# Kernel tuning notes

Measured on AMD Instinct MI355X. Metric: run time of the kernel, lower is better.

## Reference

```python
import jax, jax.numpy as jnp
import numpy as np

DIM = 1024
HEADS = 16
HEAD_DIM = DIM // HEADS
SCALE = HEAD_DIM ** -0.5


def setup_inputs() -> dict:
    key = jax.random.key(0)
    ks = jax.random.split(key, 6)
    B, N, C = 2, 2048, DIM
    q = jax.random.normal(ks[0], (B, N, C), dtype=jnp.float32)
    k = jax.random.normal(ks[1], (B, N, C), dtype=jnp.float32)
    v = jax.random.normal(ks[2], (B, N, C), dtype=jnp.float32)
    # torch nn.Linear weights: out = x @ W.T (+ b); qkv has no bias (qkv_bias=False)
    W_qkv = jax.random.normal(ks[3], (3 * C, 3 * C), dtype=jnp.float32) * (3 * C) ** -0.5
    W_proj = jax.random.normal(ks[4], (C, C), dtype=jnp.float32) * C ** -0.5
    b_proj = jax.random.normal(ks[5], (C,), dtype=jnp.float32) * 0.02
    return {"q": q, "k": k, "v": v, "W_qkv": W_qkv, "W_proj": W_proj, "b_proj": b_proj}


def reference(q, k, v, W_qkv, W_proj, b_proj):
    B, N, C = q.shape
    # fused QKV projection on concatenated [q,k,v] -> [B,N,3C]
    qkv = jnp.concatenate([q, k, v], axis=-1) @ W_qkv.T
    qkv = qkv.reshape(B, N, 3, HEADS, HEAD_DIM).transpose(2, 0, 3, 1, 4)  # [3,B,H,N,hd]
    qh, kh, vh = qkv[0], qkv[1], qkv[2]
    attn = jnp.einsum('bhqd,bhkd->bhqk', qh, kh) * SCALE
    attn = jax.nn.softmax(attn, axis=-1)  # attn_drop is identity (p=0)
    x = jnp.einsum('bhqk,bhkd->bhqd', attn, vh)  # [B,H,N,hd]
    x = x.transpose(0, 2, 1, 3).reshape(B, N, C)
    x = x @ W_proj.T + b_proj  # proj_drop is identity (p=0)
    return x
```

## Files before the change

### kernel.cpp

```cpp
#include <hip/hip_runtime.h>
#include <hip/hip_bf16.h>
#include <stdint.h>

#define HEADS 16
#define HD 64
#define SEQ 2048
#define BATCH 2
#define CDIM 1024
#define MROWS (BATCH*SEQ)
#define K3C (3*CDIM)
#define ATT_SCALE 0.125f

typedef __bf16 bf16x8 __attribute__((ext_vector_type(8)));
typedef float  f32x4  __attribute__((ext_vector_type(4)));

__device__ __forceinline__ unsigned short f2bf(float f) {
    __hip_bfloat16 h = __float2bfloat16(f);
    return __builtin_bit_cast(unsigned short, h);
}
__device__ __forceinline__ unsigned int pack2bf(float a, float b) {
    return (unsigned int)f2bf(a) | ((unsigned int)f2bf(b) << 16);
}
__device__ __forceinline__ bf16x8 frag(uint4 u) { return __builtin_bit_cast(bf16x8, u); }

__device__ __forceinline__ void async16(const unsigned short* g, unsigned short* lds) {
    __builtin_amdgcn_global_load_lds(
        (const __attribute__((address_space(1))) unsigned int*)g,
        (__attribute__((address_space(3))) unsigned int*)lds, 16, 0, 0);
}

__global__ void cast_all(const float* __restrict__ q, const float* __restrict__ k,
                         const float* __restrict__ v, const float* __restrict__ Wq,
                         const float* __restrict__ Wp,
                         unsigned short* __restrict__ A, unsigned short* __restrict__ Wqb,
                         unsigned short* __restrict__ Wpb)
{
    const int bid = blockIdx.x;
    const int t = threadIdx.x;
    if (bid < MROWS) {
        const float* srcs[3] = {q, k, v};
        #pragma unroll
        for (int i = 0; i < 3; ++i) {
            float4 f = *(const float4*)(srcs[i] + (size_t)bid*CDIM + t*4);
            ushort4 s;
            s.x = f2bf(f.x); s.y = f2bf(f.y); s.z = f2bf(f.z); s.w = f2bf(f.w);
            *(ushort4*)(A + (size_t)bid*K3C + i*CDIM + t*4) = s;
        }
    } else if (bid < MROWS + 9216) {
        int idx = (bid - MROWS)*256 + t;
        float4 f = ((const float4*)Wq)[idx];
        ushort4 s;
        s.x = f2bf(f.x); s.y = f2bf(f.y); s.z = f2bf(f.z); s.w = f2bf(f.w);
        ((ushort4*)Wqb)[idx] = s;
    } else {
        int idx = (bid - MROWS - 9216)*256 + t;
        float4 f = ((const float4*)Wp)[idx];
        ushort4 s;
        s.x = f2bf(f.x); s.y = f2bf(f.y); s.z = f2bf(f.z); s.w = f2bf(f.w);
        ((ushort4*)Wpb)[idx] = s;
    }
}

template<int EPI>
__global__ __launch_bounds__(256, 2)
void gemm_bt(const unsigned short* __restrict__ A, const unsigned short* __restrict__ B,
             int M, int N, int K,
             unsigned short* __restrict__ qh, unsigned short* __restrict__ kh,
             unsigned short* __restrict__ vt,
             const float* __restrict__ bias, float* __restrict__ out)
{
    __shared__ __attribute__((aligned(16))) unsigned short As[128*32];
    __shared__ __attribute__((aligned(16))) unsigned short Bs[128*32];
    const int tid  = threadIdx.x;
    const int wave = tid >> 6;
    const int lane = tid & 63;
    const int l15  = lane & 15;
    const int quad = lane >> 4;
    const int wm = (wave >> 1) * 64;
    const int wn = (wave & 1) * 64;
    const int m0 = blockIdx.x * 128;
    const int n0 = blockIdx.y * 128;

    f32x4 acc[4][4] = {};

    const int srow = tid >> 2;
    const int sc8  = (tid & 3) * 8;

    for (int k0 = 0; k0 < K; k0 += 32) {
        #pragma unroll
        for (int t = 0; t < 2; ++t) {
            int row = t*64 + srow;
            const unsigned short* ga = A + (size_t)(m0 + row)*K + k0 + sc8;
            const unsigned short* gb = B + (size_t)(n0 + row)*K + k0 + sc8;
            async16(ga, &As[(t*256 + wave*64)*8]);
            async16(gb, &Bs[(t*256 + wave*64)*8]);
        }
        __syncthreads();
        uint4 af[4], bfv[4];
        #pragma unroll
        for (int i = 0; i < 4; ++i) {
            af[i]  = *(const uint4*)&As[(wm + i*16 + l15)*32 + quad*8];
            bfv[i] = *(const uint4*)&Bs[(wn + i*16 + l15)*32 + quad*8];
        }
        #pragma unroll
        for (int mi = 0; mi < 4; ++mi)
            #pragma unroll
            for (int ni = 0; ni < 4; ++ni)
                acc[mi][ni] = __builtin_amdgcn_mfma_f32_16x16x32_bf16(
                    frag(af[mi]), frag(bfv[ni]), acc[mi][ni], 0, 0, 0);
        __syncthreads();
    }

    if constexpr (EPI == 0) {
        #pragma unroll
        for (int mi = 0; mi < 4; ++mi) {
            int row0 = m0 + wm + mi*16 + quad*4;
            int b  = row0 >> 11;
            int nq = row0 & 2047;
            #pragma unroll
            for (int ni = 0; ni < 4; ++ni) {
                int col   = n0 + wn + ni*16 + l15;
                int which = col >> 10;
                int h     = (col >> 6) & 15;
                int d     = col & 63;
                int bh    = b*HEADS + h;
                if (which == 2) {
                    ushort4 pv;
                    pv.x = f2bf(acc[mi][ni][0]);
                    pv.y = f2bf(acc[mi][ni][1]);
                    pv.z = f2bf(acc[mi][ni][2]);
                    pv.w = f2bf(acc[mi][ni][3]);
                    *(ushort4*)&vt[((size_t)bh*HD + d)*SEQ + nq] = pv;
                } else {
                    unsigned short* dst = (which == 0) ? qh : kh;
                    float sc = (which == 0) ? ATT_SCALE : 1.0f;
                    #pragma unroll
                    for (int r = 0; r < 4; ++r)
                        dst[((size_t)bh*SEQ + nq + r)*HD + d] = f2bf(acc[mi][ni][r] * sc);
                }
            }
        }
    } else {
        #pragma unroll
        for (int mi = 0; mi < 4; ++mi) {
            int row0 = m0 + wm + mi*16 + quad*4;
            #pragma unroll
            for (int ni = 0; ni < 4; ++ni) {
                int col  = n0 + wn + ni*16 + l15;
                float bv = bias[col];
                #pragma unroll
                for (int r = 0; r < 4; ++r)
                    out[(size_t)(row0 + r)*N + col] = acc[mi][ni][r] + bv;
            }
        }
    }
}

__global__ __launch_bounds__(256, 2)
void attention(const unsigned short* __restrict__ qh, const unsigned short* __restrict__ kh,
               const unsigned short* __restrict__ vt, unsigned short* __restrict__ xb)
{
    const int qt = blockIdx.x;
    const int h  = blockIdx.y;
    const int b  = blockIdx.z;
    const int bh = b*HEADS + h;
    const int tid  = threadIdx.x;
    const int wave = tid >> 6;
    const int lane = tid & 63;
    const int l15  = lane & 15;
    const int quad = lane >> 4;

    __shared__ __attribute__((aligned(16))) unsigned short Ks[2][64*64];
    __shared__ __attribute__((aligned(16))) unsigned short Vs[2][64*64];
    __shared__ __attribute__((aligned(16))) unsigned short Ps[4][16*72];

    const unsigned short* Qp = qh + ((size_t)bh*SEQ + qt*64)*HD;
    const unsigned short* Kp = kh + (size_t)bh*SEQ*HD;
    const unsigned short* Vp = vt + (size_t)bh*HD*SEQ;

    auto stage = [&](int kt, int bufI) {
        #pragma unroll
        for (int t = 0; t < 2; ++t) {
            int c  = t*256 + wave*64 + lane;
            int r  = c >> 3;
            int cc = (c & 7) ^ (r & 7);
            async16(Kp + (size_t)(kt*64 + r)*HD + cc*8,
                    &Ks[bufI][(t*256 + wave*64)*8]);
            async16(Vp + (size_t)r*SEQ + kt*64 + cc*8,
                    &Vs[bufI][(t*256 + wave*64)*8]);
        }
    };

    uint4 qf0 = *(const uint4*)(Qp + (size_t)(wave*16 + l15)*HD + quad*8);
    uint4 qf1 = *(const uint4*)(Qp + (size_t)(wave*16 + l15)*HD + 32 + quad*8);

    f32x4 o[4] = {};
    float m_s = -INFINITY, l_s = 0.f;

    unsigned short* Pl = Ps[wave];
    const int x7 = l15 & 7;

    stage(0, 0);

    for (int kt = 0; kt < SEQ/64; ++kt) {
        stage((kt + 1) & 31, (kt + 1) & 1);
        asm volatile("s_waitcnt vmcnt(4)" ::: "memory");
        asm volatile("s_barrier" ::: "memory");

        const unsigned short* Kb = Ks[kt & 1];
        const unsigned short* Vb = Vs[kt & 1];

        f32x4 s[4];
        #pragma unroll
        for (int st = 0; st < 4; ++st) {
            int rb = st*16 + l15;
            uint4 kf0 = *(const uint4*)&Kb[(rb*8 + (quad ^ x7))*8];
            uint4 kf1 = *(const uint4*)&Kb[(rb*8 + ((4 + quad) ^ x7))*8];
            f32x4 z = {};
            z = __builtin_amdgcn_mfma_f32_16x16x32_bf16(frag(kf0), frag(qf0), z, 0, 0, 0);
            z = __builtin_amdgcn_mfma_f32_16x16x32_bf16(frag(kf1), frag(qf1), z, 0, 0, 0);
            s[st] = z;
        }

        float mloc = s[0][0];
        #pragma unroll
        for (int st = 0; st < 4; ++st)
            #pragma unroll
            for (int r = 0; r < 4; ++r)
                mloc = fmaxf(mloc, s[st][r]);
        mloc = fmaxf(mloc, __shfl_xor(mloc, 16));
        mloc = fmaxf(mloc, __shfl_xor(mloc, 32));

        float mn = fmaxf(m_s, mloc);
        float al = __expf(m_s - mn);
        m_s = mn;

        float p[4][4];
        float rs = 0.f;
        #pragma unroll
        for (int st = 0; st < 4; ++st)
            #pragma unroll
            for (int r = 0; r < 4; ++r) { p[st][r] = __expf(s[st][r] - mn); rs += p[st][r]; }
        rs += __shfl_xor(rs, 16);
        rs += __shfl_xor(rs, 32);
        l_s = al*l_s + rs;

        #pragma unroll
        for (int st = 0; st < 4; ++st)
            #pragma unroll
            for (int r = 0; r < 4; ++r)
                o[st][r] *= al;

        #pragma unroll
        for (int st = 0; st < 4; ++st) {
            uint2 pk;
            pk.x = pack2bf(p[st][0], p[st][1]);
            pk.y = pack2bf(p[st][2], p[st][3]);
            *(uint2*)&Pl[l15*72 + st*16 + quad*4] = pk;
        }
        asm volatile("s_waitcnt lgkmcnt(0)" ::: "memory");

        uint4 pB0 = *(const uint4*)&Pl[l15*72 + quad*8];
        uint4 pB1 = *(const uint4*)&Pl[l15*72 + 32 + quad*8];

        #pragma unroll
        for (int st = 0; st < 4; ++st) {
            int rb = st*16 + l15;
            uint4 vf0 = *(const uint4*)&Vb[(rb*8 + (quad ^ x7))*8];
            uint4 vf1 = *(const uint4*)&Vb[(rb*8 + ((4 + quad) ^ x7))*8];
            o[st] = __builtin_amdgcn_mfma_f32_16x16x32_bf16(frag(vf0), frag(pB0), o[st], 0, 0, 0);
            o[st] = __builtin_amdgcn_mfma_f32_16x16x32_bf16(frag(vf1), frag(pB1), o[st], 0, 0, 0);
        }

        asm volatile("s_barrier" ::: "memory");
    }

    float inv = 1.0f / l_s;
    #pragma unroll
    for (int st = 0; st < 4; ++st) {
        uint2 pk;
        pk.x = pack2bf(o[st][0]*inv, o[st][1]*inv);
        pk.y = pack2bf(o[st][2]*inv, o[st][3]*inv);
        *(uint2*)&Pl[l15*72 + st*16 + quad*4] = pk;
    }
    asm volatile("s_waitcnt lgkmcnt(0)" ::: "memory");
    __syncthreads();

    const int qr = lane >> 2;
    const int dd = (lane & 3) * 16;
    uint4 oa = *(const uint4*)&Pl[qr*72 + dd];
    uint4 ob = *(const uint4*)&Pl[qr*72 + dd + 8];
    const int mrow = b*SEQ + qt*64 + wave*16 + qr;
    *(uint4*)&xb[(size_t)mrow*CDIM + h*HD + dd]     = oa;
    *(uint4*)&xb[(size_t)mrow*CDIM + h*HD + dd + 8] = ob;
}

extern "C" void kernel_launch(void* const* d_in, const int* in_sizes, int n_in,
                              void* d_out, int out_size, void* d_ws, size_t ws_size,
                              hipStream_t stream)
{
    const float* q  = (const float*)d_in[0];
    const float* k  = (const float*)d_in[1];
    const float* v  = (const float*)d_in[2];
    const float* Wq = (const float*)d_in[3];
    const float* Wp = (const float*)d_in[4];
    const float* bp = (const float*)d_in[5];
    float* out = (float*)d_out;

    char* p = (char*)d_ws;
    auto carve = [&](size_t bytes) { char* r = p; p += (bytes + 255) & ~(size_t)255; return r; };
    unsigned short* Abuf   = (unsigned short*)carve((size_t)MROWS*K3C*2);
    unsigned short* Wqkvb  = (unsigned short*)carve((size_t)K3C*K3C*2);
    unsigned short* Wprojb = (unsigned short*)carve((size_t)CDIM*CDIM*2);
    unsigned short* qhb    = (unsigned short*)carve((size_t)BATCH*HEADS*SEQ*HD*2);
    unsigned short* khb    = (unsigned short*)carve((size_t)BATCH*HEADS*SEQ*HD*2);
    unsigned short* vtb    = (unsigned short*)carve((size_t)BATCH*HEADS*SEQ*HD*2);
    unsigned short* xbuf   = (unsigned short*)carve((size_t)MROWS*CDIM*2);

    cast_all<<<MROWS + 9216 + 1024, 256, 0, stream>>>(q, k, v, Wq, Wp, Abuf, Wqkvb, Wprojb);

    gemm_bt<0><<<dim3(MROWS/128, K3C/128), 256, 0, stream>>>(
        Abuf, Wqkvb, MROWS, K3C, K3C, qhb, khb, vtb, nullptr, nullptr);

    attention<<<dim3(SEQ/64, HEADS, BATCH), 256, 0, stream>>>(qhb, khb, vtb, xbuf);

    gemm_bt<1><<<dim3(MROWS/128, CDIM/128), 256, 0, stream>>>(
        xbuf, Wprojb, MROWS, CDIM, CDIM, nullptr, nullptr, nullptr, bp, out);
}
```

Baseline: 314.5 us.

## Process 128 query rows per attention block with exp2 softmax

Each wave now handles two 16-row query groups, so a block covers 128 queries and reuses every staged K/V tile twice. This halves K/V global traffic and LDS fragment reads per query. The softmax scale is folded with log2(e) into Q so exp2 can replace expf. The final __syncthreads is dropped because each wave only reads back its own LDS region. In exchange, register pressure rises and the grid is halved to 512 blocks, which may reduce occupancy.

```diff
diff --git a/kernel.cpp b/kernel.cpp
--- a/kernel.cpp
+++ b/kernel.cpp
@@ -9,7 +9,7 @@
 #define CDIM 1024
 #define MROWS (BATCH*SEQ)
 #define K3C (3*CDIM)
-#define ATT_SCALE 0.125f
+#define QSCALE 0.1803368801111244f
 
 typedef __bf16 bf16x8 __attribute__((ext_vector_type(8)));
 typedef float  f32x4  __attribute__((ext_vector_type(4)));
@@ -133,7 +133,7 @@
                     *(ushort4*)&vt[((size_t)bh*HD + d)*SEQ + nq] = pv;
                 } else {
                     unsigned short* dst = (which == 0) ? qh : kh;
-                    float sc = (which == 0) ? ATT_SCALE : 1.0f;
+                    float sc = (which == 0) ? QSCALE : 1.0f;
                     #pragma unroll
                     for (int r = 0; r < 4; ++r)
                         dst[((size_t)bh*SEQ + nq + r)*HD + d] = f2bf(acc[mi][ni][r] * sc);
@@ -172,9 +172,9 @@
 
     __shared__ __attribute__((aligned(16))) unsigned short Ks[2][64*64];
     __shared__ __attribute__((aligned(16))) unsigned short Vs[2][64*64];
-    __shared__ __attribute__((aligned(16))) unsigned short Ps[4][16*72];
-
-    const unsigned short* Qp = qh + ((size_t)bh*SEQ + qt*64)*HD;
+    __shared__ __attribute__((aligned(16))) unsigned short Ps[4][2*16*72];
+
+    const unsigned short* Qp = qh + ((size_t)bh*SEQ + qt*128 + wave*32)*HD;
     const unsigned short* Kp = kh + (size_t)bh*SEQ*HD;
     const unsigned short* Vp = vt + (size_t)bh*HD*SEQ;
 
@@ -191,16 +191,21 @@
         }
     };
 
-    uint4 qf0 = *(const uint4*)(Qp + (size_t)(wave*16 + l15)*HD + quad*8);
-    uint4 qf1 = *(const uint4*)(Qp + (size_t)(wave*16 + l15)*HD + 32 + quad*8);
-
-    f32x4 o[4] = {};
-    float m_s = -INFINITY, l_s = 0.f;
-
-    unsigned short* Pl = Ps[wave];
+    stage(0, 0);
+
+    uint4 qf[2][2];
+    #pragma unroll
+    for (int g = 0; g < 2; ++g) {
+        qf[g][0] = *(const uint4*)(Qp + (size_t)(g*16 + l15)*HD + quad*8);
+        qf[g][1] = *(const uint4*)(Qp + (size_t)(g*16 + l15)*HD + 32 + quad*8);
+    }
+
+    f32x4 o[2][4] = {};
+    float m_s[2] = {-INFINITY, -INFINITY};
+    float l_s[2] = {0.f, 0.f};
+
+    unsigned short* Pw = Ps[wave];
     const int x7 = l15 & 7;
-
-    stage(0, 0);
 
     for (int kt = 0; kt < SEQ/64; ++kt) {
         stage((kt + 1) & 31, (kt + 1) & 1);
@@ -210,89 +215,110 @@
         const unsigned short* Kb = Ks[kt & 1];
         const unsigned short* Vb = Vs[kt & 1];
 
-        f32x4 s[4];
+        f32x4 s[2][4];
         #pragma unroll
         for (int st = 0; st < 4; ++st) {
             int rb = st*16 + l15;
             uint4 kf0 = *(const uint4*)&Kb[(rb*8 + (quad ^ x7))*8];
             uint4 kf1 = *(const uint4*)&Kb[(rb*8 + ((4 + quad) ^ x7))*8];
-            f32x4 z = {};
-            z = __builtin_amdgcn_mfma_f32_16x16x32_bf16(frag(kf0), frag(qf0), z, 0, 0, 0);
-            z = __builtin_amdgcn_mfma_f32_16x16x32_bf16(frag(kf1), frag(qf1), z, 0, 0, 0);
-            s[st] = z;
-        }
-
-        float mloc = s[0][0];
-        #pragma unroll
-        for (int st = 0; st < 4; ++st)
-            #pragma unroll
-            for (int r = 0; r < 4; ++r)
-                mloc = fmaxf(mloc, s[st][r]);
-        mloc = fmaxf(mloc, __shfl_xor(mloc, 16));
-        mloc = fmaxf(mloc, __shfl_xor(mloc, 32));
-
-        float mn = fmaxf(m_s, mloc);
-        float al = __expf(m_s - mn);
-        m_s = mn;
-
-        float p[4][4];
-        float rs = 0.f;
-        #pragma unroll
-        for (int st = 0; st < 4; ++st)
-            #pragma unroll
-            for (int r = 0; r < 4; ++r) { p[st][r] = __expf(s[st][r] - mn); rs += p[st][r]; }
-        rs += __shfl_xor(rs, 16);
-        rs += __shfl_xor(rs, 32);
-        l_s = al*l_s + rs;
-
-        #pragma unroll
-        for (int st = 0; st < 4; ++st)
-            #pragma unroll
-            for (int r = 0; r < 4; ++r)
-                o[st][r] *= al;
-
-        #pragma unroll
-        for (int st = 0; st < 4; ++st) {
-            uint2 pk;
-            pk.x = pack2bf(p[st][0], p[st][1]);
-            pk.y = pack2bf(p[st][2], p[st][3]);
-            *(uint2*)&Pl[l15*72 + st*16 + quad*4] = pk;
+            #pragma unroll
+            for (int g = 0; g < 2; ++g) {
+                f32x4 z = {};
+                z = __builtin_amdgcn_mfma_f32_16x16x32_bf16(frag(kf0), frag(qf[g][0]), z, 0, 0, 0);
+                z = __builtin_amdgcn_mfma_f32_16x16x32_bf16(frag(kf1), frag(qf[g][1]), z, 0, 0, 0);
+                s[g][st] = z;
+            }
+        }
+
+        #pragma unroll
+        for (int g = 0; g < 2; ++g) {
+            float mloc = s[g][0][0];
+            #pragma unroll
+            for (int st = 0; st < 4; ++st)
+                #pragma unroll
+                for (int r = 0; r < 4; ++r)
+                    mloc = fmaxf(mloc, s[g][st][r]);
+            mloc = fmaxf(mloc, __shfl_xor(mloc, 16));
+            mloc = fmaxf(mloc, __shfl_xor(mloc, 32));
+
+            float mn = fmaxf(m_s[g], mloc);
+            float al = __builtin_amdgcn_exp2f(m_s[g] - mn);
+            m_s[g] = mn;
+
+            float rs = 0.f;
+            float p[4][4];
+            #pragma unroll
+            for (int st = 0; st < 4; ++st)
+                #pragma unroll
+                for (int r = 0; r < 4; ++r) {
+                    p[st][r] = __builtin_amdgcn_exp2f(s[g][st][r] - mn);
+                    rs += p[st][r];
+                }
+            rs += __shfl_xor(rs, 16);
+            rs += __shfl_xor(rs, 32);
+            l_s[g] = al*l_s[g] + rs;
+
+            #pragma unroll
+            for (int st = 0; st < 4; ++st)
+                #pragma unroll
+                for (int r = 0; r < 4; ++r)
+                    o[g][st][r] *= al;
+
+            #pragma unroll
+            for (int st = 0; st < 4; ++st) {
+                uint2 pk;
+                pk.x = pack2bf(p[st][0], p[st][1]);
+                pk.y = pack2bf(p[st][2], p[st][3]);
+                *(uint2*)&Pw[g*1152 + l15*72 + st*16 + quad*4] = pk;
+            }
         }
         asm volatile("s_waitcnt lgkmcnt(0)" ::: "memory");
 
-        uint4 pB0 = *(const uint4*)&Pl[l15*72 + quad*8];
-        uint4 pB1 = *(const uint4*)&Pl[l15*72 + 32 + quad*8];
+        uint4 pB[2][2];
+        #pragma unroll
+        for (int g = 0; g < 2; ++g) {
+            pB[g][0] = *(const uint4*)&Pw[g*1152 + l15*72 + quad*8];
+            pB[g][1] = *(const uint4*)&Pw[g*1152 + l15*72 + 32 + quad*8];
+        }
 
         #pragma unroll
         for (int st = 0; st < 4; ++st) {
             int rb = st*16 + l15;
             uint4 vf0 = *(const uint4*)&Vb[(rb*8 + (quad ^ x7))*8];
             uint4 vf1 = *(const uint4*)&Vb[(rb*8 + ((4 + quad) ^ x7))*8];
-            o[st] = __builtin_amdgcn_mfma_f32_16x16x32_bf16(frag(vf0), frag(pB0), o[st], 0, 0, 0);
-            o[st] = __builtin_amdgcn_mfma_f32_16x16x32_bf16(frag(vf1), frag(pB1), o[st], 0, 0, 0);
+            #pragma unroll
+            for (int g = 0; g < 2; ++g) {
+                o[g][st] = __builtin_amdgcn_mfma_f32_16x16x32_bf16(frag(vf0), frag(pB[g][0]), o[g][st], 0, 0, 0);
+                o[g][st] = __builtin_amdgcn_mfma_f32_16x16x32_bf16(frag(vf1), frag(pB[g][1]), o[g][st], 0, 0, 0);
+            }
         }
 
         asm volatile("s_barrier" ::: "memory");
     }
 
-    float inv = 1.0f / l_s;
     #pragma unroll
-    for (int st = 0; st < 4; ++st) {
-        uint2 pk;
-        pk.x = pack2bf(o[st][0]*inv, o[st][1]*inv);
-        pk.y = pack2bf(o[st][2]*inv, o[st][3]*inv);
-        *(uint2*)&Pl[l15*72 + st*16 + quad*4] = pk;
+    for (int g = 0; g < 2; ++g) {
+        float inv = 1.0f / l_s[g];
+        #pragma unroll
+        for (int st = 0; st < 4; ++st) {
+            uint2 pk;
+            pk.x = pack2bf(o[g][st][0]*inv, o[g][st][1]*inv);
+            pk.y = pack2bf(o[g][st][2]*inv, o[g][st][3]*inv);
+            *(uint2*)&Pw[g*1152 + l15*72 + st*16 + quad*4] = pk;
+        }
     }
     asm volatile("s_waitcnt lgkmcnt(0)" ::: "memory");
-    __syncthreads();
 
     const int qr = lane >> 2;
     const int dd = (lane & 3) * 16;
-    uint4 oa = *(const uint4*)&Pl[qr*72 + dd];
-    uint4 ob = *(const uint4*)&Pl[qr*72 + dd + 8];
-    const int mrow = b*SEQ + qt*64 + wave*16 + qr;
-    *(uint4*)&xb[(size_t)mrow*CDIM + h*HD + dd]     = oa;
-    *(uint4*)&xb[(size_t)mrow*CDIM + h*HD + dd + 8] = ob;
+    #pragma unroll
+    for (int g = 0; g < 2; ++g) {
+        uint4 oa = *(const uint4*)&Pw[g*1152 + qr*72 + dd];
+        uint4 ob = *(const uint4*)&Pw[g*1152 + qr*72 + dd + 8];
+        const int mrow = b*SEQ + qt*128 + wave*32 + g*16 + qr;
+        *(uint4*)&xb[(size_t)mrow*CDIM + h*HD + dd]     = oa;
+        *(uint4*)&xb[(size_t)mrow*CDIM + h*HD + dd + 8] = ob;
+    }
 }
 
 extern "C" void kernel_launch(void* const* d_in, const int* in_sizes, int n_in,
@@ -322,7 +348,7 @@
     gemm_bt<0><<<dim3(MROWS/128, K3C/128), 256, 0, stream>>>(
         Abuf, Wqkvb, MROWS, K3C, K3C, qhb, khb, vtb, nullptr, nullptr);
 
-    attention<<<dim3(SEQ/64, HEADS, BATCH), 256, 0, stream>>>(qhb, khb, vtb, xbuf);
+    attention<<<dim3(SEQ/128, HEADS, BATCH), 256, 0, stream>>>(qhb, khb, vtb, xbuf);
 
     gemm_bt<1><<<dim3(MROWS/128, CDIM/128), 256, 0, stream>>>(
         xbuf, Wprojb, MROWS, CDIM, CDIM, nullptr, nullptr, nullptr, bp, out);
```

New measurement: 302.2 us. -3.9%, faster.
